# Optimization experiments

Measured on AMD Instinct MI355X. Metric: run time of the kernel, lower is better.

The kernel has to match this reference:

```python
import jax, jax.numpy as jnp
import numpy as np

B, C, H, W = 32, 512, 56, 56


def setup_inputs() -> dict:
    key = jax.random.key(0)
    k1, k2, k3 = jax.random.split(key, 3)
    x = jax.random.normal(k1, (B, C, H, W), dtype=jnp.float32)
    scale = 1.0 / np.sqrt(C)  # kaiming-ish init for bias-free Linear(C, C)
    W1 = jax.random.normal(k2, (C, C), dtype=jnp.float32) * scale  # fc (sigmoid gate)
    W3 = jax.random.normal(k3, (C, C), dtype=jnp.float32) * scale  # fc3 (relu gate)
    return {"x": x, "W1": W1, "W3": W3}


def reference(x, W1, W3):
    x = jax.nn.relu(x)
    # Stage 1: peak-vs-avg region suppression (per (b,c) spatial reductions)
    avg_region = jnp.mean(x, axis=(2, 3), keepdims=True)   # [B,C,1,1]
    peak_region = jnp.max(x, axis=(2, 3), keepdims=True)   # [B,C,1,1]
    x = jnp.where((peak_region - avg_region) < 0.5, 0.0, x)
    # Stage 2: channel max/mean exp-based gating
    cmax = jnp.max(x, axis=1, keepdims=True)               # [B,1,H,W]
    cmean = jnp.mean(x, axis=1, keepdims=True)             # [B,1,H,W]
    bb = 1.0 - jnp.exp(-jnp.abs(cmax - cmean))
    x = bb * x
    # Stage 3: max extractor
    x_max = jnp.max(x, axis=(2, 3), keepdims=True)         # [B,C,1,1]
    # Stages 4-5: suppression controllers (global avg pool -> FC gates)
    pooled = jnp.mean(x, axis=(2, 3))                      # [B,C]
    control1 = jax.nn.sigmoid(pooled @ W1.T)[:, :, None, None]
    control3 = jax.nn.relu(pooled @ W3.T)
    control3 = jnp.where(control3 < 1.0, 1.2, control3)[:, :, None, None]
    thres = control1 * control3 * x_max                    # [B,C,1,1]
    return jnp.where(x < thres, 0.0, x)
```

## Files before the change

### kernel.cpp

```cpp
#include <hip/hip_runtime.h>

#define NB 32
#define NC 512
#define NH 56
#define NW 56
#define HW 3136
#define CHW 1605632
#define CPB 16
#define NPART 32

__global__ __launch_bounds__(256) void k12_maskbb(const float* __restrict__ x,
                                                  float* __restrict__ mask,
                                                  float* __restrict__ pmax,
                                                  double* __restrict__ psum) {
    const int b = blockIdx.x >> 5;
    const int ch = blockIdx.x & 31;
    const int c0 = ch * CPB;
    const int tid = threadIdx.x;
    __shared__ double rsum[4];
    __shared__ float rmax[4];
    const bool has4 = (tid < 16);
    float am[16];
    double as[16];
#pragma unroll
    for (int k = 0; k < 16; k++) { am[k] = 0.f; as[k] = 0.0; }

    for (int p = 0; p < CPB; p++) {
        const float4* px = (const float4*)(x + (size_t)(b * NC + c0 + p) * HW);
        float v[16];
#pragma unroll
        for (int k = 0; k < 4; k++) {
            if (k < 3 || has4) {
                float4 t = px[tid + k * 256];
                v[4 * k + 0] = fmaxf(t.x, 0.f);
                v[4 * k + 1] = fmaxf(t.y, 0.f);
                v[4 * k + 2] = fmaxf(t.z, 0.f);
                v[4 * k + 3] = fmaxf(t.w, 0.f);
            } else {
                v[4 * k + 0] = 0.f; v[4 * k + 1] = 0.f;
                v[4 * k + 2] = 0.f; v[4 * k + 3] = 0.f;
            }
        }
        float lmax = 0.f;
        double lsum = 0.0;
#pragma unroll
        for (int k = 0; k < 16; k++) {
            lmax = fmaxf(lmax, v[k]);
            lsum += (double)v[k];
        }
        for (int off = 32; off; off >>= 1) {
            lsum += __shfl_xor(lsum, off);
            lmax = fmaxf(lmax, __shfl_xor(lmax, off));
        }
        __syncthreads();
        if ((tid & 63) == 0) { rsum[tid >> 6] = lsum; rmax[tid >> 6] = lmax; }
        __syncthreads();
        double s = rsum[0] + rsum[1] + rsum[2] + rsum[3];
        float m = fmaxf(fmaxf(rmax[0], rmax[1]), fmaxf(rmax[2], rmax[3]));
        float avg = (float)(s / 3136.0);
        float mk = ((m - avg) < 0.5f) ? 0.f : 1.f;
        if (tid == 0) mask[b * NC + c0 + p] = mk;
        if (mk != 0.f) {
#pragma unroll
            for (int k = 0; k < 16; k++) {
                am[k] = fmaxf(am[k], v[k]);
                as[k] += (double)v[k];
            }
        }
    }
    const size_t pb = ((size_t)ch * NB + b) * HW;
#pragma unroll
    for (int k = 0; k < 4; k++) {
        if (k < 3 || has4) {
            const int pos = 4 * (tid + k * 256);
            *(float4*)(pmax + pb + pos) =
                make_float4(am[4 * k], am[4 * k + 1], am[4 * k + 2], am[4 * k + 3]);
            *(double2*)(psum + pb + pos)     = make_double2(as[4 * k],     as[4 * k + 1]);
            *(double2*)(psum + pb + pos + 2) = make_double2(as[4 * k + 2], as[4 * k + 3]);
        }
    }
}

__global__ __launch_bounds__(256) void k2bb_fin(const float* __restrict__ pmax,
                                                const double* __restrict__ psum,
                                                float* __restrict__ bb) {
    const int i = blockIdx.x * 256 + threadIdx.x;
    const int b = i / HW, pos = i % HW;
    float m = 0.f;
    double s = 0.0;
#pragma unroll 4
    for (int ch = 0; ch < NPART; ch++) {
        const size_t idx = ((size_t)ch * NB + b) * HW + pos;
        m = fmaxf(m, pmax[idx]);
        s += psum[idx];
    }
    double cmean = s * (1.0 / 512.0);
    double d = fabs((double)m - cmean);
    bb[i] = (float)(1.0 - exp(-d));
}

__global__ __launch_bounds__(256) void k2b_stats(const float* __restrict__ x,
                                                 const float* __restrict__ mask,
                                                 const float* __restrict__ bb,
                                                 float* __restrict__ xmax,
                                                 float* __restrict__ pooled) {
    const int plane = blockIdx.x;
    const int b = plane >> 9;
    const float4* px = (const float4*)(x + (size_t)plane * HW);
    const float4* pbb = (const float4*)(bb + (size_t)b * HW);
    const float mk = mask[plane];
    float m = 0.f;
    double s = 0.0;
    for (int i = threadIdx.x; i < HW / 4; i += 256) {
        float4 v = px[i];
        float4 bv = pbb[i];
        float x0 = fmaxf(v.x, 0.f) * mk * bv.x;
        float x1 = fmaxf(v.y, 0.f) * mk * bv.y;
        float x2 = fmaxf(v.z, 0.f) * mk * bv.z;
        float x3 = fmaxf(v.w, 0.f) * mk * bv.w;
        m = fmaxf(m, fmaxf(fmaxf(x0, x1), fmaxf(x2, x3)));
        s += (double)x0 + (double)x1 + (double)x2 + (double)x3;
    }
    for (int off = 32; off; off >>= 1) {
        s += __shfl_xor(s, off);
        m = fmaxf(m, __shfl_xor(m, off));
    }
    __shared__ double ssum[4];
    __shared__ float smax[4];
    int wid = threadIdx.x >> 6, lane = threadIdx.x & 63;
    if (lane == 0) { ssum[wid] = s; smax[wid] = m; }
    __syncthreads();
    if (threadIdx.x == 0) {
        double st = ssum[0] + ssum[1] + ssum[2] + ssum[3];
        float mt = fmaxf(fmaxf(smax[0], smax[1]), fmaxf(smax[2], smax[3]));
        xmax[plane] = mt;
        pooled[plane] = (float)(st / 3136.0);
    }
}

__global__ __launch_bounds__(256) void k3_gates(const float* __restrict__ pooled,
                                                const float* __restrict__ W1,
                                                const float* __restrict__ W3,
                                                const float* __restrict__ xmax,
                                                float* __restrict__ thres) {
    int wave = threadIdx.x >> 6, lane = threadIdx.x & 63;
    int task0 = (blockIdx.x * 4 + wave) * 4;
    for (int t = 0; t < 4; t++) {
        int task = task0 + t;
        int b = task >> 9, j = task & 511;
        const float* r1 = W1 + j * 512;
        const float* r3 = W3 + j * 512;
        const float* pr = pooled + b * 512;
        double s1 = 0.0, s3 = 0.0;
        for (int k = lane; k < 512; k += 64) {
            double p = (double)pr[k];
            s1 += p * (double)r1[k];
            s3 += p * (double)r3[k];
        }
        for (int off = 32; off; off >>= 1) {
            s1 += __shfl_xor(s1, off);
            s3 += __shfl_xor(s3, off);
        }
        if (lane == 0) {
            float c1 = (float)(1.0 / (1.0 + exp(-s1)));
            double r = s3 > 0.0 ? s3 : 0.0;
            float c3 = (float)((r < 1.0) ? 1.2 : r);
            thres[task] = c1 * c3 * xmax[task];
        }
    }
}

__global__ __launch_bounds__(256) void k4_out(const float* __restrict__ x,
                                              const float* __restrict__ mask,
                                              const float* __restrict__ bb,
                                              const float* __restrict__ thres,
                                              float* __restrict__ out) {
    const int plane = blockIdx.x;
    const int b = plane >> 9;
    const float4* px = (const float4*)(x + (size_t)plane * HW);
    float4* po = (float4*)(out + (size_t)plane * HW);
    const float4* pbb = (const float4*)(bb + (size_t)b * HW);
    const float th = thres[plane];
    const float mk = mask[plane];
    for (int i = threadIdx.x; i < HW / 4; i += 256) {
        float4 v = px[i];
        float4 bv = pbb[i];
        float x0 = fmaxf(v.x, 0.f) * mk * bv.x;
        float x1 = fmaxf(v.y, 0.f) * mk * bv.y;
        float x2 = fmaxf(v.z, 0.f) * mk * bv.z;
        float x3 = fmaxf(v.w, 0.f) * mk * bv.w;
        float4 o;
        o.x = (x0 < th) ? 0.f : x0;
        o.y = (x1 < th) ? 0.f : x1;
        o.z = (x2 < th) ? 0.f : x2;
        o.w = (x3 < th) ? 0.f : x3;
        po[i] = o;
    }
}

extern "C" void kernel_launch(void* const* d_in, const int* in_sizes, int n_in,
                              void* d_out, int out_size, void* d_ws, size_t ws_size,
                              hipStream_t stream) {
    const float* x  = (const float*)d_in[0];
    const float* W1 = (const float*)d_in[1];
    const float* W3 = (const float*)d_in[2];
    float* out = (float*)d_out;
    float* ws = (float*)d_ws;
    float* bb     = ws;
    float* mask   = ws + 100352;
    float* xmax   = ws + 116736;
    float* pooled = ws + 133120;
    float* thres  = ws + 149504;
    double* psum = (double*)d_out;
    float* pmax  = (float*)d_out + NPART * NB * HW * 2;

    hipLaunchKernelGGL(k12_maskbb, dim3(NB * NPART),    dim3(256), 0, stream,
                       x, mask, pmax, psum);
    hipLaunchKernelGGL(k2bb_fin,   dim3(NB * HW / 256), dim3(256), 0, stream,
                       pmax, psum, bb);
    hipLaunchKernelGGL(k2b_stats,  dim3(NB * NC), dim3(256), 0, stream,
                       x, mask, bb, xmax, pooled);
    hipLaunchKernelGGL(k3_gates,   dim3(1024),    dim3(256), 0, stream,
                       pooled, W1, W3, xmax, thres);
    hipLaunchKernelGGL(k4_out,     dim3(NB * NC), dim3(256), 0, stream,
                       x, mask, bb, thres, out);
}
```

Baseline: 449.0 us.

## Split mask computation into its own per-plane kernel before channel partials

The fused mask+partial kernel is split in two. A new per-plane kernel computes the region mask, and a separate partial-reduction kernel reads that mask and accumulates channel max/sum without any per-channel block barriers. The number of channel groups per batch drops from 32 to 16, each covering 32 channels, and the channel loop is unrolled by 2. This removes two __syncthreads per channel from the serial loop, but it adds a full extra read of x (about 205MB) and halves the block count of the partial kernel, which lowers parallelism.

```diff
diff --git a/kernel.cpp b/kernel.cpp
--- a/kernel.cpp
+++ b/kernel.cpp
@@ -6,65 +6,74 @@
 #define NW 56
 #define HW 3136
 #define CHW 1605632
-#define CPB 16
-#define NPART 32
-
-__global__ __launch_bounds__(256) void k12_maskbb(const float* __restrict__ x,
-                                                  float* __restrict__ mask,
-                                                  float* __restrict__ pmax,
-                                                  double* __restrict__ psum) {
-    const int b = blockIdx.x >> 5;
-    const int ch = blockIdx.x & 31;
+#define CPB 32
+#define NPART 16
+
+__global__ __launch_bounds__(256) void k1_mask(const float* __restrict__ x,
+                                               float* __restrict__ mask) {
+    const int plane = blockIdx.x;
+    const float4* px = (const float4*)(x + (size_t)plane * HW);
+    float lmax = 0.f;
+    double lsum = 0.0;
+    for (int i = threadIdx.x; i < HW / 4; i += 256) {
+        float4 v = px[i];
+        float f0 = fmaxf(v.x, 0.f), f1 = fmaxf(v.y, 0.f);
+        float f2 = fmaxf(v.z, 0.f), f3 = fmaxf(v.w, 0.f);
+        lmax = fmaxf(lmax, fmaxf(fmaxf(f0, f1), fmaxf(f2, f3)));
+        lsum += (double)f0 + (double)f1 + (double)f2 + (double)f3;
+    }
+    for (int off = 32; off; off >>= 1) {
+        lsum += __shfl_xor(lsum, off);
+        lmax = fmaxf(lmax, __shfl_xor(lmax, off));
+    }
+    __shared__ double ssum[4];
+    __shared__ float smax[4];
+    int wid = threadIdx.x >> 6, lane = threadIdx.x & 63;
+    if (lane == 0) { ssum[wid] = lsum; smax[wid] = lmax; }
+    __syncthreads();
+    if (threadIdx.x == 0) {
+        double s = ssum[0] + ssum[1] + ssum[2] + ssum[3];
+        float m = fmaxf(fmaxf(smax[0], smax[1]), fmaxf(smax[2], smax[3]));
+        float avg = (float)(s / 3136.0);
+        mask[plane] = ((m - avg) < 0.5f) ? 0.f : 1.f;
+    }
+}
+
+__global__ __launch_bounds__(256) void k2p_part(const float* __restrict__ x,
+                                                const float* __restrict__ mask,
+                                                float* __restrict__ pmax,
+                                                double* __restrict__ psum) {
+    const int b = blockIdx.x >> 4;
+    const int ch = blockIdx.x & 15;
     const int c0 = ch * CPB;
     const int tid = threadIdx.x;
-    __shared__ double rsum[4];
-    __shared__ float rmax[4];
     const bool has4 = (tid < 16);
     float am[16];
     double as[16];
 #pragma unroll
     for (int k = 0; k < 16; k++) { am[k] = 0.f; as[k] = 0.0; }
 
+#pragma unroll 2
     for (int p = 0; p < CPB; p++) {
-        const float4* px = (const float4*)(x + (size_t)(b * NC + c0 + p) * HW);
-        float v[16];
+        const int c = c0 + p;
+        const float mk = mask[b * NC + c];
+        const float4* px = (const float4*)(x + (size_t)(b * NC + c) * HW);
 #pragma unroll
         for (int k = 0; k < 4; k++) {
             if (k < 3 || has4) {
                 float4 t = px[tid + k * 256];
-                v[4 * k + 0] = fmaxf(t.x, 0.f);
-                v[4 * k + 1] = fmaxf(t.y, 0.f);
-                v[4 * k + 2] = fmaxf(t.z, 0.f);
-                v[4 * k + 3] = fmaxf(t.w, 0.f);
-            } else {
-                v[4 * k + 0] = 0.f; v[4 * k + 1] = 0.f;
-                v[4 * k + 2] = 0.f; v[4 * k + 3] = 0.f;
-            }
-        }
-        float lmax = 0.f;
-        double lsum = 0.0;
-#pragma unroll
-        for (int k = 0; k < 16; k++) {
-            lmax = fmaxf(lmax, v[k]);
-            lsum += (double)v[k];
-        }
-        for (int off = 32; off; off >>= 1) {
-            lsum += __shfl_xor(lsum, off);
-            lmax = fmaxf(lmax, __shfl_xor(lmax, off));
-        }
-        __syncthreads();
-        if ((tid & 63) == 0) { rsum[tid >> 6] = lsum; rmax[tid >> 6] = lmax; }
-        __syncthreads();
-        double s = rsum[0] + rsum[1] + rsum[2] + rsum[3];
-        float m = fmaxf(fmaxf(rmax[0], rmax[1]), fmaxf(rmax[2], rmax[3]));
-        float avg = (float)(s / 3136.0);
-        float mk = ((m - avg) < 0.5f) ? 0.f : 1.f;
-        if (tid == 0) mask[b * NC + c0 + p] = mk;
-        if (mk != 0.f) {
-#pragma unroll
-            for (int k = 0; k < 16; k++) {
-                am[k] = fmaxf(am[k], v[k]);
-                as[k] += (double)v[k];
+                float f0 = fmaxf(t.x, 0.f) * mk;
+                float f1 = fmaxf(t.y, 0.f) * mk;
+                float f2 = fmaxf(t.z, 0.f) * mk;
+                float f3 = fmaxf(t.w, 0.f) * mk;
+                am[4 * k + 0] = fmaxf(am[4 * k + 0], f0);
+                am[4 * k + 1] = fmaxf(am[4 * k + 1], f1);
+                am[4 * k + 2] = fmaxf(am[4 * k + 2], f2);
+                am[4 * k + 3] = fmaxf(am[4 * k + 3], f3);
+                as[4 * k + 0] += (double)f0;
+                as[4 * k + 1] += (double)f1;
+                as[4 * k + 2] += (double)f2;
+                as[4 * k + 3] += (double)f3;
             }
         }
     }
@@ -212,9 +221,10 @@
     float* pooled = ws + 133120;
     float* thres  = ws + 149504;
     double* psum = (double*)d_out;
-    float* pmax  = (float*)d_out + NPART * NB * HW * 2;
-
-    hipLaunchKernelGGL(k12_maskbb, dim3(NB * NPART),    dim3(256), 0, stream,
+    float* pmax  = (float*)d_out + (size_t)NPART * NB * HW * 2;
+
+    hipLaunchKernelGGL(k1_mask,    dim3(NB * NC),       dim3(256), 0, stream, x, mask);
+    hipLaunchKernelGGL(k2p_part,   dim3(NB * NPART),    dim3(256), 0, stream,
                        x, mask, pmax, psum);
     hipLaunchKernelGGL(k2bb_fin,   dim3(NB * HW / 256), dim3(256), 0, stream,
                        pmax, psum, bb);
```

Result: slower. 465.9 us (+3.8%).

## Fuse all five phases into one cooperative persistent kernel with grid syncs

Applied to the files above, without the earlier changes.

Merges the five separate kernels into a single cooperative launch of 1024 blocks that separates the phases with grid-wide syncs. Plane-wise phases loop over planes with a grid stride. The aim is to remove kernel launch gaps and the tail effects between phases. In exchange, the plane phases run on a fixed grid of 1024 blocks, which may lower memory-level parallelism, and each grid sync has its own cost. A fallback runs the original multi-kernel path if the cooperative launch fails.

```diff
diff --git a/kernel.cpp b/kernel.cpp
--- a/kernel.cpp
+++ b/kernel.cpp
@@ -1,22 +1,24 @@
 #include <hip/hip_runtime.h>
+#include <hip/hip_cooperative_groups.h>
+
+namespace cg = cooperative_groups;
 
 #define NB 32
 #define NC 512
 #define NH 56
 #define NW 56
 #define HW 3136
-#define CHW 1605632
 #define CPB 16
 #define NPART 32
-
-__global__ __launch_bounds__(256) void k12_maskbb(const float* __restrict__ x,
-                                                  float* __restrict__ mask,
-                                                  float* __restrict__ pmax,
-                                                  double* __restrict__ psum) {
-    const int b = blockIdx.x >> 5;
-    const int ch = blockIdx.x & 31;
+#define GRID 1024
+
+
+__device__ __forceinline__ void ph1_maskpart(const float* __restrict__ x,
+                                             float* mask, float* pmax, double* psum,
+                                             int bid, int tid) {
+    const int b = bid >> 5;
+    const int ch = bid & 31;
     const int c0 = ch * CPB;
-    const int tid = threadIdx.x;
     __shared__ double rsum[4];
     __shared__ float rmax[4];
     const bool has4 = (tid < 16);
@@ -81,10 +83,8 @@
     }
 }
 
-__global__ __launch_bounds__(256) void k2bb_fin(const float* __restrict__ pmax,
-                                                const double* __restrict__ psum,
-                                                float* __restrict__ bb) {
-    const int i = blockIdx.x * 256 + threadIdx.x;
+__device__ __forceinline__ void ph2_bbfin(const float* pmax, const double* psum,
+                                          float* bb, int i) {
     const int b = i / HW, pos = i % HW;
     float m = 0.f;
     double s = 0.0;
@@ -99,19 +99,17 @@
     bb[i] = (float)(1.0 - exp(-d));
 }
 
-__global__ __launch_bounds__(256) void k2b_stats(const float* __restrict__ x,
-                                                 const float* __restrict__ mask,
-                                                 const float* __restrict__ bb,
-                                                 float* __restrict__ xmax,
-                                                 float* __restrict__ pooled) {
-    const int plane = blockIdx.x;
+__device__ __forceinline__ void ph3_stats(const float* __restrict__ x,
+                                          const float* mask, const float* bb,
+                                          float* xmax, float* pooled,
+                                          int plane, int tid) {
     const int b = plane >> 9;
     const float4* px = (const float4*)(x + (size_t)plane * HW);
     const float4* pbb = (const float4*)(bb + (size_t)b * HW);
     const float mk = mask[plane];
     float m = 0.f;
     double s = 0.0;
-    for (int i = threadIdx.x; i < HW / 4; i += 256) {
+    for (int i = tid; i < HW / 4; i += 256) {
         float4 v = px[i];
         float4 bv = pbb[i];
         float x0 = fmaxf(v.x, 0.f) * mk * bv.x;
@@ -127,24 +125,25 @@
     }
     __shared__ double ssum[4];
     __shared__ float smax[4];
-    int wid = threadIdx.x >> 6, lane = threadIdx.x & 63;
+    int wid = tid >> 6, lane = tid & 63;
     if (lane == 0) { ssum[wid] = s; smax[wid] = m; }
     __syncthreads();
-    if (threadIdx.x == 0) {
+    if (tid == 0) {
         double st = ssum[0] + ssum[1] + ssum[2] + ssum[3];
         float mt = fmaxf(fmaxf(smax[0], smax[1]), fmaxf(smax[2], smax[3]));
         xmax[plane] = mt;
         pooled[plane] = (float)(st / 3136.0);
     }
-}
-
-__global__ __launch_bounds__(256) void k3_gates(const float* __restrict__ pooled,
-                                                const float* __restrict__ W1,
-                                                const float* __restrict__ W3,
-                                                const float* __restrict__ xmax,
-                                                float* __restrict__ thres) {
-    int wave = threadIdx.x >> 6, lane = threadIdx.x & 63;
-    int task0 = (blockIdx.x * 4 + wave) * 4;
+    __syncthreads();
+}
+
+__device__ __forceinline__ void ph4_gates(const float* pooled,
+                                          const float* __restrict__ W1,
+                                          const float* __restrict__ W3,
+                                          const float* xmax, float* thres,
+                                          int bid, int tid) {
+    int wave = tid >> 6, lane = tid & 63;
+    int task0 = (bid * 4 + wave) * 4;
     for (int t = 0; t < 4; t++) {
         int task = task0 + t;
         int b = task >> 9, j = task & 511;
@@ -170,19 +169,17 @@
     }
 }
 
-__global__ __launch_bounds__(256) void k4_out(const float* __restrict__ x,
-                                              const float* __restrict__ mask,
-                                              const float* __restrict__ bb,
-                                              const float* __restrict__ thres,
-                                              float* __restrict__ out) {
-    const int plane = blockIdx.x;
+__device__ __forceinline__ void ph5_out(const float* __restrict__ x,
+                                        const float* mask, const float* bb,
+                                        const float* thres, float* out,
+                                        int plane, int tid) {
     const int b = plane >> 9;
     const float4* px = (const float4*)(x + (size_t)plane * HW);
     float4* po = (float4*)(out + (size_t)plane * HW);
     const float4* pbb = (const float4*)(bb + (size_t)b * HW);
     const float th = thres[plane];
     const float mk = mask[plane];
-    for (int i = threadIdx.x; i < HW / 4; i += 256) {
+    for (int i = tid; i < HW / 4; i += 256) {
         float4 v = px[i];
         float4 bv = pbb[i];
         float x0 = fmaxf(v.x, 0.f) * mk * bv.x;
@@ -196,6 +193,47 @@
         o.w = (x3 < th) ? 0.f : x3;
         po[i] = o;
     }
+}
+
+__global__ __launch_bounds__(256, 4) void k_all(const float* __restrict__ x,
+                                                const float* __restrict__ W1,
+                                                const float* __restrict__ W3,
+                                                float* out, float* mask, float* bb,
+                                                float* xmax, float* pooled, float* thres,
+                                                float* pmax, double* psum) {
+    cg::grid_group g = cg::this_grid();
+    const int bid = blockIdx.x, tid = threadIdx.x;
+
+    ph1_maskpart(x, mask, pmax, psum, bid, tid);
+    g.sync();
+    if (bid < NB * HW / 256) ph2_bbfin(pmax, psum, bb, bid * 256 + tid);
+    g.sync();
+    for (int pl = bid; pl < NB * NC; pl += GRID) ph3_stats(x, mask, bb, xmax, pooled, pl, tid);
+    g.sync();
+    ph4_gates(pooled, W1, W3, xmax, thres, bid, tid);
+    g.sync();
+    for (int pl = bid; pl < NB * NC; pl += GRID) ph5_out(x, mask, bb, thres, out, pl, tid);
+}
+
+__global__ __launch_bounds__(256) void k12_s(const float* __restrict__ x, float* mask,
+                                             float* pmax, double* psum) {
+    ph1_maskpart(x, mask, pmax, psum, blockIdx.x, threadIdx.x);
+}
+__global__ __launch_bounds__(256) void k2bb_s(const float* pmax, const double* psum, float* bb) {
+    ph2_bbfin(pmax, psum, bb, blockIdx.x * 256 + threadIdx.x);
+}
+__global__ __launch_bounds__(256) void k2b_s(const float* __restrict__ x, const float* mask,
+                                             const float* bb, float* xmax, float* pooled) {
+    ph3_stats(x, mask, bb, xmax, pooled, blockIdx.x, threadIdx.x);
+}
+__global__ __launch_bounds__(256) void k3_s(const float* pooled, const float* __restrict__ W1,
+                                            const float* __restrict__ W3, const float* xmax,
+                                            float* thres) {
+    ph4_gates(pooled, W1, W3, xmax, thres, blockIdx.x, threadIdx.x);
+}
+__global__ __launch_bounds__(256) void k4_s(const float* __restrict__ x, const float* mask,
+                                            const float* bb, const float* thres, float* out) {
+    ph5_out(x, mask, bb, thres, out, blockIdx.x, threadIdx.x);
 }
 
 extern "C" void kernel_launch(void* const* d_in, const int* in_sizes, int n_in,
@@ -212,16 +250,19 @@
     float* pooled = ws + 133120;
     float* thres  = ws + 149504;
     double* psum = (double*)d_out;
-    float* pmax  = (float*)d_out + NPART * NB * HW * 2;
-
-    hipLaunchKernelGGL(k12_maskbb, dim3(NB * NPART),    dim3(256), 0, stream,
-                       x, mask, pmax, psum);
-    hipLaunchKernelGGL(k2bb_fin,   dim3(NB * HW / 256), dim3(256), 0, stream,
-                       pmax, psum, bb);
-    hipLaunchKernelGGL(k2b_stats,  dim3(NB * NC), dim3(256), 0, stream,
-                       x, mask, bb, xmax, pooled);
-    hipLaunchKernelGGL(k3_gates,   dim3(1024),    dim3(256), 0, stream,
-                       pooled, W1, W3, xmax, thres);
-    hipLaunchKernelGGL(k4_out,     dim3(NB * NC), dim3(256), 0, stream,
-                       x, mask, bb, thres, out);
-}
+    float* pmax  = (float*)d_out + (size_t)NPART * NB * HW * 2;
+
+    void* args[] = {(void*)&x, (void*)&W1, (void*)&W3, (void*)&out, (void*)&mask,
+                    (void*)&bb, (void*)&xmax, (void*)&pooled, (void*)&thres,
+                    (void*)&pmax, (void*)&psum};
+    hipError_t e = hipLaunchCooperativeKernel((const void*)k_all, dim3(GRID), dim3(256),
+                                              args, 0, stream);
+    if (e != hipSuccess) {
+        (void)hipGetLastError();
+        hipLaunchKernelGGL(k12_s,  dim3(NB * NPART),    dim3(256), 0, stream, x, mask, pmax, psum);
+        hipLaunchKernelGGL(k2bb_s, dim3(NB * HW / 256), dim3(256), 0, stream, pmax, psum, bb);
+        hipLaunchKernelGGL(k2b_s,  dim3(NB * NC),       dim3(256), 0, stream, x, mask, bb, xmax, pooled);
+        hipLaunchKernelGGL(k3_s,   dim3(1024),          dim3(256), 0, stream, pooled, W1, W3, xmax, thres);
+        hipLaunchKernelGGL(k4_s,   dim3(NB * NC),       dim3(256), 0, stream, x, mask, bb, thres, out);
+    }
+}
```

Measured after the change: 934.0 us. 2.08x slower.
